# Kernel tuning notes

Measured on AMD Instinct MI355X. Metric: run time of the kernel, lower is better.

The kernel has to match this reference:

```python
import jax, jax.numpy as jnp
import numpy as np

C = 512
GROUPS = 32
EPS = 1e-6


def setup_inputs() -> dict:
    key = jax.random.key(0)
    ks = jax.random.split(key, 10)
    s = 0.02
    return {
        "x": jax.random.normal(ks[0], (2, C, 64, 64), dtype=jnp.float32),
        "gn_scale": jnp.ones((C,), jnp.float32),
        "gn_bias": jnp.zeros((C,), jnp.float32),
        "wq": jax.random.normal(ks[1], (C, C), jnp.float32) * s,
        "bq": jnp.zeros((C,), jnp.float32),
        "wk": jax.random.normal(ks[2], (C, C), jnp.float32) * s,
        "bk": jnp.zeros((C,), jnp.float32),
        "wv": jax.random.normal(ks[3], (C, C), jnp.float32) * s,
        "bv": jnp.zeros((C,), jnp.float32),
        "wo": jax.random.normal(ks[4], (C, C), jnp.float32) * s,
        "bo": jnp.zeros((C,), jnp.float32),
    }


def group_norm(x, scale, bias):
    # x: [b, c, h, w]; 32 groups over channel dim
    b, c, h, w = x.shape
    xg = x.reshape(b, GROUPS, c // GROUPS, h, w)
    mean = jnp.mean(xg, axis=(2, 3, 4), keepdims=True)
    var = jnp.var(xg, axis=(2, 3, 4), keepdims=True)
    xg = (xg - mean) * jax.lax.rsqrt(var + EPS)
    x = xg.reshape(b, c, h, w)
    return x * scale[None, :, None, None] + bias[None, :, None, None]


def reference(x, gn_scale, gn_bias, wq, bq, wk, bk, wv, bv, wo, bo):
    b, c, h, w = x.shape
    n = h * w
    hn = group_norm(x, gn_scale, gn_bias).reshape(b, c, n)  # [b,c,n]
    # 1x1 conv == channel matmul: out[b,o,n] = W[o,i] @ h[b,i,n] + bias
    q = jnp.einsum('oi,bin->bon', wq, hn) + bq[None, :, None]
    k = jnp.einsum('oi,bin->bon', wk, hn) + bk[None, :, None]
    v = jnp.einsum('oi,bin->bon', wv, hn) + bv[None, :, None]
    # weight[b, i, j] = q_i . k_j, softmax over j
    scale = int(c) ** (-0.5)
    weight = jnp.einsum('bci,bcj->bij', q, k) * scale  # [b,n,n]
    weight = jax.nn.softmax(weight, axis=2)
    # h[b,c,i] = sum_j v[b,c,j] * weight[b,i,j]
    out = jnp.einsum('bcj,bij->bci', v, weight)
    out = jnp.einsum('oi,bin->bon', wo, out) + bo[None, :, None]
    return out.reshape(b, c, h, w) + x
```

## Files before the change

### kernel.cpp

```cpp
#include <hip/hip_runtime.h>
#include <hip/hip_bf16.h>


typedef __attribute__((ext_vector_type(8))) short short8_t;
typedef __attribute__((ext_vector_type(4))) short short4_t;
typedef __attribute__((ext_vector_type(4))) float f32x4;

__device__ __forceinline__ void gload16(const void* g, void* l) {
  __builtin_amdgcn_global_load_lds(
      (const __attribute__((address_space(1))) void*)g,
      (__attribute__((address_space(3))) void*)l, 16, 0, 0);
}

__device__ __forceinline__ short f2bf_bits(float f) {
  __hip_bfloat16 h = __float2bfloat16(f);
  return *reinterpret_cast<short*>(&h);
}
__device__ __forceinline__ float bfbits2f(short s) {
  union { unsigned int u; float f; } c;
  c.u = ((unsigned int)(unsigned short)s) << 16;
  return c.f;
}

template<int OUTF, int BIASMODE, int RESID, int PIPE, int SWZ, int MF>
__global__ __launch_bounds__(256, 2)
void gemm_nt(const __hip_bfloat16* __restrict__ A,
             const __hip_bfloat16* __restrict__ B,
             void* __restrict__ Cv,
             const float* __restrict__ bias,
             const float* __restrict__ resid,
             float scale, int M, int N, int K,
             int lda, int ldb, int ldc,
             long long strA, long long strB, long long strC, long long strR)
{
  int bm, bn, bz;
  if (SWZ == 0) {
    bm = blockIdx.x; bn = blockIdx.y; bz = blockIdx.z;
  } else if (SWZ == 2) {
    const int b = blockIdx.x;
    bz = b >> 10;
    const int b2 = b & 1023;
    const int xcd = b2 & 7, s = b2 >> 3;
    bm = (xcd >> 1) * 8 + (s & 7);
    bn = (xcd & 1) * 16 + (s >> 3);
  } else {
    const int b = blockIdx.x;
    const int xcd = b & 7, slot = b >> 3;
    bm = slot & 7;
    const int panel = xcd * 8 + (slot >> 3);
    bn = panel & 31; bz = panel >> 5;
  }
  const int z = bz;
  A += (size_t)z * strA;
  B += (size_t)z * strB;

  const int tid = threadIdx.x;
  const int w = tid >> 6, l = tid & 63;
  const int wr = w >> 1, wc = w & 1;
  const int lhi = l >> 4, llo = l & 15;
  const int m0 = bm * (MF * 32), n0 = bn * 128;

  constexpr int BUFSZ = MF * 4096 + 16384;
  __shared__ char sm[(PIPE ? 2 : 1) * BUFSZ];

  f32x4 acc[MF][4] = {};

  const int rowInCh = l >> 3;
  const int colOff = 8 * ((l & 7) ^ (rowInCh & 7));

  const __hip_bfloat16* gAr[MF];
  const __hip_bfloat16* gBr[4];
#pragma unroll
  for (int j = 0; j < MF; ++j)
    gAr[j] = A + (size_t)(m0 + w * (8 * MF) + j * 8 + rowInCh) * lda + colOff;
#pragma unroll
  for (int r = 0; r < 4; ++r)
    gBr[r] = B + (size_t)(n0 + w * 32 + r * 8 + rowInCh) * ldb + colOff;

  auto stage = [&](int kt, int buf) {
    char* sA = sm + buf * BUFSZ;
    char* sB = sA + MF * 4096;
    const int ko = kt * 64;
#pragma unroll
    for (int j = 0; j < MF; ++j)
      gload16(gAr[j] + ko, sA + (w * MF + j) * 1024);
#pragma unroll
    for (int r = 0; r < 4; ++r)
      gload16(gBr[r] + ko, sB + (w * 4 + r) * 1024);
  };

  auto compute = [&](int buf) {
    char* sA = sm + buf * BUFSZ;
    char* sB = sA + MF * 4096;
#pragma unroll
    for (int kk = 0; kk < 2; ++kk) {
      short8_t af[MF], bf[4];
#pragma unroll
      for (int m = 0; m < MF; ++m) {
        const int row = wr * (16 * MF) + m * 16 + llo;
        const int inner = ((kk * 4 + lhi) ^ (row & 7)) * 16;
        af[m] = *(const short8_t*)(sA + row * 128 + inner);
      }
#pragma unroll
      for (int n = 0; n < 4; ++n) {
        const int row = wc * 64 + n * 16 + llo;
        const int inner = ((kk * 4 + lhi) ^ (row & 7)) * 16;
        bf[n] = *(const short8_t*)(sB + row * 128 + inner);
      }
#pragma unroll
      for (int m = 0; m < MF; ++m)
#pragma unroll
        for (int n = 0; n < 4; ++n)
          acc[m][n] = __builtin_amdgcn_mfma_f32_16x16x32_bf16(af[m], bf[n], acc[m][n], 0, 0, 0);
    }
  };

  const int nkt = K >> 6;
  if (PIPE) {
    stage(0, 0);
    __syncthreads();
    int cur = 0;
    for (int kt = 0; kt < nkt; ++kt) {
      if (kt + 1 < nkt) stage(kt + 1, cur ^ 1);
      compute(cur);
      __syncthreads();
      cur ^= 1;
    }
  } else {
    for (int kt = 0; kt < nkt; ++kt) {
      __syncthreads();
      stage(kt, 0);
      __syncthreads();
      compute(0);
    }
  }

#pragma unroll
  for (int m = 0; m < MF; ++m) {
#pragma unroll
    for (int r = 0; r < 4; ++r) {
      const int grow = m0 + wr * (16 * MF) + m * 16 + lhi * 4 + r;
#pragma unroll
      for (int n = 0; n < 4; ++n) {
        const int gcol = n0 + wc * 64 + n * 16 + llo;
        float v = acc[m][n][r] * scale;
        if (BIASMODE == 1) v += bias[grow];
        if (BIASMODE == 2) v += bias[gcol];
        const size_t idx = (size_t)z * strC + (size_t)grow * ldc + gcol;
        if (RESID) v += resid[(size_t)z * strR + (size_t)grow * ldc + gcol];
        if (OUTF == 0) ((__hip_bfloat16*)Cv)[idx] = __float2bfloat16(v);
        else           ((float*)Cv)[idx] = v;
      }
    }
  }
}

__global__ __launch_bounds__(256)
void gn_partial(const float* __restrict__ x, float* __restrict__ part)
{
  const int g = blockIdx.x, sl = blockIdx.y, z = blockIdx.z;
  const int tid = threadIdx.x;
  const float* xf = x + (size_t)z * 512 * 4096 + (size_t)g * 16 * 4096 + (size_t)sl * 4096;
  const float4* px = reinterpret_cast<const float4*>(xf);
  float s = 0.f, q = 0.f;
#pragma unroll
  for (int i = 0; i < 4; ++i) {
    float4 v = px[tid + i * 256];
    s += v.x + v.y + v.z + v.w;
    q += v.x * v.x + v.y * v.y + v.z * v.z + v.w * v.w;
  }
#pragma unroll
  for (int o = 32; o; o >>= 1) { s += __shfl_xor(s, o); q += __shfl_xor(q, o); }
  __shared__ float rs[4], rq[4];
  if ((tid & 63) == 0) { rs[tid >> 6] = s; rq[tid >> 6] = q; }
  __syncthreads();
  if (tid == 0) {
    s = rs[0] + rs[1] + rs[2] + rs[3];
    q = rq[0] + rq[1] + rq[2] + rq[3];
    part[(((size_t)z * 32 + g) * 16 + sl) * 2 + 0] = s;
    part[(((size_t)z * 32 + g) * 16 + sl) * 2 + 1] = q;
  }
}

__global__ __launch_bounds__(64)
void gn_finalize(const float* __restrict__ part, float* __restrict__ stats, int n)
{
  const int i = threadIdx.x;
  if (i >= n) return;
  float s = 0.f, q = 0.f;
#pragma unroll
  for (int sl = 0; sl < 16; ++sl) {
    s += part[(i * 16 + sl) * 2 + 0];
    q += part[(i * 16 + sl) * 2 + 1];
  }
  const float mean = s * (1.0f / 65536.0f);
  const float var = q * (1.0f / 65536.0f) - mean * mean;
  stats[i * 2 + 0] = mean;
  stats[i * 2 + 1] = rsqrtf(var + 1e-6f);
}

__global__ __launch_bounds__(256)
void gn_apply_t(const float* __restrict__ x, const float* __restrict__ stats,
                const float* __restrict__ gns, const float* __restrict__ gnb,
                __hip_bfloat16* __restrict__ ht)
{
  const int st = blockIdx.x, ct = blockIdx.y, z = blockIdx.z;
  const int tid = threadIdx.x;
  __shared__ float tile[64][65];
  const float* xb = x + (size_t)z * 512 * 4096;
  const int lane64 = tid & 63, rr = tid >> 6;
#pragma unroll
  for (int pp = 0; pp < 16; ++pp) {
    const int cl = pp * 4 + rr;
    const int c = ct * 64 + cl;
    const int g = c >> 4;
    const float mean = stats[(z * 32 + g) * 2 + 0];
    const float rstd = stats[(z * 32 + g) * 2 + 1];
    const float val = xb[(size_t)c * 4096 + st * 64 + lane64];
    tile[cl][lane64] = (val - mean) * rstd * gns[c] + gnb[c];
  }
  __syncthreads();
  __hip_bfloat16* hb = ht + (size_t)z * 4096 * 512;
#pragma unroll
  for (int pp = 0; pp < 16; ++pp) {
    const int sl = pp * 4 + rr;
    const int s = st * 64 + sl;
    hb[(size_t)s * 512 + ct * 64 + lane64] = __float2bfloat16(tile[lane64][sl]);
  }
}

__global__ __launch_bounds__(256)
void softmax_rows(__hip_bfloat16* __restrict__ S, long long strZ)
{
  const int row = blockIdx.x, z = blockIdx.y;
  __hip_bfloat16* p = S + (size_t)z * strZ + (size_t)row * 4096;
  const int tid = threadIdx.x;
  short8_t a = *(const short8_t*)(p + tid * 16);
  short8_t b = *(const short8_t*)(p + tid * 16 + 8);
  float v[16];
#pragma unroll
  for (int i = 0; i < 8; ++i) { v[i] = bfbits2f(a[i]); v[8 + i] = bfbits2f(b[i]); }
  float m = v[0];
#pragma unroll
  for (int i = 1; i < 16; ++i) m = fmaxf(m, v[i]);
#pragma unroll
  for (int o = 32; o; o >>= 1) m = fmaxf(m, __shfl_xor(m, o));
  __shared__ float red[8];
  if ((tid & 63) == 0) red[tid >> 6] = m;
  __syncthreads();
  m = fmaxf(fmaxf(red[0], red[1]), fmaxf(red[2], red[3]));
  float s = 0.f;
#pragma unroll
  for (int i = 0; i < 16; ++i) { v[i] = exp2f((v[i] - m) * 1.44269504f); s += v[i]; }
#pragma unroll
  for (int o = 32; o; o >>= 1) s += __shfl_xor(s, o);
  __syncthreads();
  if ((tid & 63) == 0) red[4 + (tid >> 6)] = s;
  __syncthreads();
  s = red[4] + red[5] + red[6] + red[7];
  const float inv = 1.f / s;
#pragma unroll
  for (int i = 0; i < 8; ++i) { a[i] = f2bf_bits(v[i] * inv); b[i] = f2bf_bits(v[8 + i] * inv); }
  *(short8_t*)(p + tid * 16) = a;
  *(short8_t*)(p + tid * 16 + 8) = b;
}

__global__ __launch_bounds__(256)
void cast3(const float* __restrict__ w0, const float* __restrict__ w1,
           const float* __restrict__ w2, __hip_bfloat16* __restrict__ out)
{
  const int j = blockIdx.y;
  const float* src = (j == 0) ? w0 : (j == 1) ? w1 : w2;
  const int i = blockIdx.x * 256 + threadIdx.x;
  float4 v = reinterpret_cast<const float4*>(src)[i];
  short4_t o;
  o[0] = f2bf_bits(v.x); o[1] = f2bf_bits(v.y);
  o[2] = f2bf_bits(v.z); o[3] = f2bf_bits(v.w);
  *reinterpret_cast<short4_t*>((short*)out + (size_t)j * 262144 + (size_t)i * 4) = o;
}

__global__ __launch_bounds__(256)
void transpose_cast(const float* __restrict__ w, __hip_bfloat16* __restrict__ wt)
{
  __shared__ float tile[64][65];
  const int ct = blockIdx.x, it = blockIdx.y;
  const int tid = threadIdx.x;
  const int lane = tid & 63, rr = tid >> 6;
#pragma unroll
  for (int p = 0; p < 16; ++p) {
    const int cl = p * 4 + rr;
    tile[cl][lane] = w[(size_t)(ct * 64 + cl) * 512 + it * 64 + lane];
  }
  __syncthreads();
#pragma unroll
  for (int p = 0; p < 16; ++p) {
    const int il = p * 4 + rr;
    wt[(size_t)(it * 64 + il) * 512 + ct * 64 + lane] = __float2bfloat16(tile[lane][il]);
  }
}

__global__ __launch_bounds__(64)
void prep_bias(const float* __restrict__ wo, const float* __restrict__ bv,
               const float* __restrict__ bo, const float* __restrict__ bq,
               const float* __restrict__ bk,
               float* __restrict__ bvo, float* __restrict__ bqk)
{
  const int o = blockIdx.x * 64 + threadIdx.x;
  const float4* row = reinterpret_cast<const float4*>(wo + (size_t)o * 512);
  const float4* b4 = reinterpret_cast<const float4*>(bv);
  float s = 0.f;
#pragma unroll 8
  for (int i = 0; i < 128; ++i) {
    float4 a = row[i], b = b4[i];
    s += a.x * b.x + a.y * b.y + a.z * b.z + a.w * b.w;
  }
  bvo[o] = s + bo[o];
  bqk[o] = bq[o];
  bqk[512 + o] = bk[o];
}

extern "C" void kernel_launch(void* const* d_in, const int* in_sizes, int n_in,
                              void* d_out, int out_size, void* d_ws, size_t ws_size,
                              hipStream_t stream)
{
  const float* x   = (const float*)d_in[0];
  const float* gns = (const float*)d_in[1];
  const float* gnb = (const float*)d_in[2];
  const float* wq  = (const float*)d_in[3];
  const float* bq  = (const float*)d_in[4];
  const float* wk  = (const float*)d_in[5];
  const float* bk  = (const float*)d_in[6];
  const float* wv  = (const float*)d_in[7];
  const float* bv  = (const float*)d_in[8];
  const float* wo  = (const float*)d_in[9];
  const float* bo  = (const float*)d_in[10];
  float* out = (float*)d_out;

  const int WB = 512 * 512;
  const long long HT  = 4096LL * 512;
  const long long QKz = 4096LL * 1024;
  const long long VOz = 512LL * 4096;
  const long long SS  = 4096LL * 4096;
  const long long CHW = 512LL * 4096;

  char* base = (char*)d_ws;
  size_t off = 0;
  auto alloc = [&](size_t b) { void* r = base + off; off = (off + b + 255) & ~(size_t)255; return r; };

  __hip_bfloat16* wbf = (__hip_bfloat16*)alloc((size_t)5 * WB * 2);
  float* bqk   = (float*)alloc(1024 * 4);
  float* bvo   = (float*)alloc(512 * 4);
  float* part  = (float*)alloc(2 * 32 * 16 * 2 * 4);
  float* stats = (float*)alloc(2 * 32 * 2 * 4);
  const size_t fixed = off;

  const size_t qkB = (size_t)2 * QKz * 2;
  const size_t voB = (size_t)2 * VOz * 2;
  const size_t sB2 = (size_t)2 * SS * 2;
  const size_t sB1 = (size_t)SS * 2;
  const int MODE = (ws_size >= fixed + qkB + voB + sB2) ? 2 : 1;

  __hip_bfloat16* qk   = (__hip_bfloat16*)alloc(qkB);
  __hip_bfloat16* vo   = (__hip_bfloat16*)alloc(voB);
  const size_t sbufB = (MODE == 2) ? sB2 : sB1;
  __hip_bfloat16* sbuf = (__hip_bfloat16*)alloc(sbufB);
  __hip_bfloat16* ht = (__hip_bfloat16*)((char*)sbuf + sbufB - (size_t)2 * HT * 2);

  __hip_bfloat16* wqk = wbf;
  __hip_bfloat16* woB = wbf + 2 * WB;
  __hip_bfloat16* wvT = wbf + 3 * WB;
  __hip_bfloat16* wvo = wbf + 4 * WB;

  const float SC = 0.04419417382415922f;

  cast3<<<dim3(256, 3), 256, 0, stream>>>(wq, wk, wo, wbf);
  transpose_cast<<<dim3(8, 8), 256, 0, stream>>>(wv, wvT);
  prep_bias<<<8, 64, 0, stream>>>(wo, bv, bo, bq, bk, bvo, bqk);
  gn_partial<<<dim3(32, 16, 2), 256, 0, stream>>>(x, part);
  gn_finalize<<<1, 64, 0, stream>>>(part, stats, 64);

  gemm_nt<0, 0, 0, 1, 0, 4><<<dim3(4, 4, 1), 256, 0, stream>>>(
      woB, wvT, wvo, nullptr, nullptr, 1.f, 512, 512, 512,
      512, 512, 512, 0, 0, 0, 0);

  gn_apply_t<<<dim3(64, 8, 2), 256, 0, stream>>>(x, stats, gns, gnb, ht);

  gemm_nt<0, 2, 0, 1, 0, 4><<<dim3(32, 8, 2), 256, 0, stream>>>(
      ht, wqk, qk, bqk, nullptr, 1.f, 4096, 1024, 512,
      512, 512, 1024, HT, 0, QKz, 0);

  gemm_nt<0, 0, 0, 1, 3, 2><<<dim3(512, 1, 1), 256, 0, stream>>>(
      wvo, ht, vo, nullptr, nullptr, 1.f, 512, 4096, 512,
      512, 512, 4096, 0, HT, VOz, 0);

  if (MODE == 2) {
    gemm_nt<0, 0, 0, 0, 2, 4><<<dim3(2048, 1, 1), 256, 0, stream>>>(
        qk, qk + 512, sbuf, nullptr, nullptr, SC, 4096, 4096, 512,
        1024, 1024, 4096, QKz, QKz, SS, 0);
    softmax_rows<<<dim3(4096, 2), 256, 0, stream>>>(sbuf, SS);
    gemm_nt<1, 1, 1, 1, 3, 2><<<dim3(512, 1, 1), 256, 0, stream>>>(
        vo, sbuf, out, bvo, x, 1.f, 512, 4096, 4096,
        4096, 4096, 4096, VOz, SS, CHW, CHW);
  } else {
    for (int z = 0; z < 2; ++z) {
      gemm_nt<0, 0, 0, 0, 0, 4><<<dim3(32, 32, 1), 256, 0, stream>>>(
          qk + (size_t)z * QKz, qk + (size_t)z * QKz + 512, sbuf, nullptr, nullptr,
          SC, 4096, 4096, 512, 1024, 1024, 4096, 0, 0, 0, 0);
      softmax_rows<<<dim3(4096, 1), 256, 0, stream>>>(sbuf, 0);
      gemm_nt<1, 1, 1, 1, 0, 2><<<dim3(8, 32, 1), 256, 0, stream>>>(
          vo + (size_t)z * VOz, sbuf, out + (size_t)z * CHW, bvo, x + (size_t)z * CHW,
          1.f, 512, 4096, 4096, 4096, 4096, 4096, 0, 0, 0, 0);
    }
  }
}
```

Baseline: 167.6 us.

## Add triple-buffered LDS pipeline with vmcnt waits and new XCD swizzle for scores GEMM

Adds a PIPE==2 mode to the GEMM that keeps three LDS buffers and prefetches two k-tiles ahead. It waits with s_waitcnt vmcnt on the outstanding async loads plus a single barrier per iteration, instead of a full sync after each compute. The QK^T scores GEMM switches from MF=4 with the old swizzle and no pipelining to MF=2 with a new XCD-aware block mapping over 4096 blocks. The aim is to hide global-to-LDS latency and improve L2 locality, at the cost of extra shared memory, which may reduce occupancy.

```diff
diff --git a/kernel.cpp b/kernel.cpp
--- a/kernel.cpp
+++ b/kernel.cpp
@@ -36,19 +36,19 @@
   int bm, bn, bz;
   if (SWZ == 0) {
     bm = blockIdx.x; bn = blockIdx.y; bz = blockIdx.z;
-  } else if (SWZ == 2) {
-    const int b = blockIdx.x;
-    bz = b >> 10;
-    const int b2 = b & 1023;
-    const int xcd = b2 & 7, s = b2 >> 3;
-    bm = (xcd >> 1) * 8 + (s & 7);
-    bn = (xcd & 1) * 16 + (s >> 3);
-  } else {
+  } else if (SWZ == 3) {
     const int b = blockIdx.x;
     const int xcd = b & 7, slot = b >> 3;
     bm = slot & 7;
     const int panel = xcd * 8 + (slot >> 3);
     bn = panel & 31; bz = panel >> 5;
+  } else {
+    const int b = blockIdx.x;
+    const int xcd = b & 7;
+    const int s = b >> 3;
+    bz = xcd >> 2;
+    bm = (xcd & 3) * 16 + (s & 15);
+    bn = s >> 4;
   }
   const int z = bz;
   A += (size_t)z * strA;
@@ -61,7 +61,9 @@
   const int m0 = bm * (MF * 32), n0 = bn * 128;
 
   constexpr int BUFSZ = MF * 4096 + 16384;
-  __shared__ char sm[(PIPE ? 2 : 1) * BUFSZ];
+  constexpr int NBUF = (PIPE == 2) ? 3 : (PIPE == 1) ? 2 : 1;
+  constexpr int LOADS = MF + 4;
+  __shared__ char sm[NBUF * BUFSZ];
 
   f32x4 acc[MF][4] = {};
 
@@ -116,7 +118,25 @@
   };
 
   const int nkt = K >> 6;
-  if (PIPE) {
+  if (PIPE == 2) {
+    stage(0, 0);
+    if (nkt > 1) stage(1, 1);
+    int cur = 0;
+    for (int kt = 0; kt < nkt; ++kt) {
+      if (kt + 1 < nkt) {
+        asm volatile("s_waitcnt vmcnt(%0)" :: "n"(LOADS) : "memory");
+      } else {
+        asm volatile("s_waitcnt vmcnt(0)" ::: "memory");
+      }
+      __builtin_amdgcn_sched_barrier(0);
+      __builtin_amdgcn_s_barrier();
+      __builtin_amdgcn_sched_barrier(0);
+      int st = cur + 2; if (st >= 3) st -= 3;
+      if (kt + 2 < nkt) stage(kt + 2, st);
+      compute(cur);
+      ++cur; if (cur == 3) cur = 0;
+    }
+  } else if (PIPE == 1) {
     stage(0, 0);
     __syncthreads();
     int cur = 0;
@@ -389,16 +409,16 @@
       ht, wqk, qk, bqk, nullptr, 1.f, 4096, 1024, 512,
       512, 512, 1024, HT, 0, QKz, 0);
 
-  gemm_nt<0, 0, 0, 1, 3, 2><<<dim3(512, 1, 1), 256, 0, stream>>>(
+  gemm_nt<0, 0, 0, 2, 3, 2><<<dim3(512, 1, 1), 256, 0, stream>>>(
       wvo, ht, vo, nullptr, nullptr, 1.f, 512, 4096, 512,
       512, 512, 4096, 0, HT, VOz, 0);
 
   if (MODE == 2) {
-    gemm_nt<0, 0, 0, 0, 2, 4><<<dim3(2048, 1, 1), 256, 0, stream>>>(
+    gemm_nt<0, 0, 0, 2, 4, 2><<<dim3(4096, 1, 1), 256, 0, stream>>>(
         qk, qk + 512, sbuf, nullptr, nullptr, SC, 4096, 4096, 512,
         1024, 1024, 4096, QKz, QKz, SS, 0);
     softmax_rows<<<dim3(4096, 2), 256, 0, stream>>>(sbuf, SS);
-    gemm_nt<1, 1, 1, 1, 3, 2><<<dim3(512, 1, 1), 256, 0, stream>>>(
+    gemm_nt<1, 1, 1, 2, 3, 2><<<dim3(512, 1, 1), 256, 0, stream>>>(
         vo, sbuf, out, bvo, x, 1.f, 512, 4096, 4096,
         4096, 4096, 4096, VOz, SS, CHW, CHW);
   } else {
```

New measurement: 173.2 us. 1.03x slower.

## Add dedicated 256x256-tile 8-wave QK^T score GEMM with phased LDS pipeline

Applied to the files above, without the earlier changes.

Replaces the generic gemm_nt call for the attention score matrix with a specialized kernel that uses 256x256 output tiles, 512 threads, a double-buffered 128KB LDS with XOR swizzle, and fine-grained phases that interleave global-to-LDS loads with MFMA work under setprio. A block index remap groups tiles by XCD for L2 locality. The larger tile cuts global traffic per FLOP. In exchange it relies on high register use, occupancy of one block per CU, and scalar bf16 stores in the epilogue.

```diff
diff --git a/kernel.cpp b/kernel.cpp
--- a/kernel.cpp
+++ b/kernel.cpp
@@ -20,6 +20,117 @@
   union { unsigned int u; float f; } c;
   c.u = ((unsigned int)(unsigned short)s) << 16;
   return c.f;
+}
+
+__global__ __launch_bounds__(512)
+void s_gemm8(const __hip_bfloat16* __restrict__ qk,
+             __hip_bfloat16* __restrict__ S, float scale)
+{
+  const long long QKz = 4096LL * 1024;
+  const long long SS  = 4096LL * 4096;
+
+  const int b = blockIdx.x;
+  const int bz = b >> 8;
+  const int r = b & 255, xcd = r & 7, sl = r >> 3;
+  const int bm = (xcd >> 1) * 4 + (sl & 3);
+  const int bn = (xcd & 1) * 8 + (sl >> 2);
+
+  const __hip_bfloat16* Aq = qk + (size_t)bz * QKz;
+  const __hip_bfloat16* Bk = Aq + 512;
+
+  const int tid = threadIdx.x;
+  const int wid = tid >> 6, l = tid & 63;
+  const int wrM = wid >> 2, wcN = wid & 3;
+  const int lhi = l >> 4, llo = l & 15;
+
+  __shared__ char sm[2 * 65536];
+
+  f32x4 acc[2][2][4][2] = {};
+
+  const int rIn = l >> 3;
+  const int colSw = 8 * ((l & 7) ^ (rIn & 7));
+  const __hip_bfloat16* gA = Aq + (size_t)(bm * 256 + rIn) * 1024 + colSw;
+  const __hip_bfloat16* gB = Bk + (size_t)(bn * 256 + rIn) * 1024 + colSw;
+
+  auto STG = [&](int mat, int half, int t) {
+    const __hip_bfloat16* src = mat ? gB : gA;
+    char* dst = sm + (t & 1) * 65536 + mat * 32768;
+    const int rb = half * 128 + wid * 16;
+    gload16(src + (size_t)rb * 1024 + t * 64, dst + rb * 128);
+    gload16(src + (size_t)(rb + 8) * 1024 + t * 64, dst + (rb + 8) * 128);
+  };
+
+#define PHASE(MH, NH, RBUF, ...) do {                                         \
+    asm volatile("s_waitcnt vmcnt(4)" ::: "memory");                          \
+    __builtin_amdgcn_sched_barrier(0);                                        \
+    short8_t af[4][2], bf[2][2];                                              \
+    const char* bbA = sm + (RBUF) * 65536;                                    \
+    const char* bbB = bbA + 32768;                                            \
+    _Pragma("unroll") for (int m = 0; m < 4; ++m) {                           \
+      const int rowA = (MH) * 128 + wrM * 64 + m * 16 + llo;                  \
+      _Pragma("unroll") for (int kk = 0; kk < 2; ++kk)                        \
+        af[m][kk] = *(const short8_t*)(bbA + rowA * 128 +                     \
+                      (((kk * 4 + lhi) ^ (rowA & 7)) * 16));                  \
+    }                                                                         \
+    _Pragma("unroll") for (int n = 0; n < 2; ++n) {                           \
+      const int rowB = (NH) * 128 + wcN * 32 + n * 16 + llo;                  \
+      _Pragma("unroll") for (int kk = 0; kk < 2; ++kk)                        \
+        bf[n][kk] = *(const short8_t*)(bbB + rowB * 128 +                     \
+                      (((kk * 4 + lhi) ^ (rowB & 7)) * 16));                  \
+    }                                                                         \
+    __VA_ARGS__;                                                              \
+    __builtin_amdgcn_sched_barrier(0);                                        \
+    __builtin_amdgcn_s_barrier();                                             \
+    __builtin_amdgcn_sched_barrier(0);                                        \
+    __builtin_amdgcn_s_setprio(1);                                            \
+    _Pragma("unroll") for (int kk = 0; kk < 2; ++kk)                          \
+      _Pragma("unroll") for (int m = 0; m < 4; ++m)                           \
+        _Pragma("unroll") for (int n = 0; n < 2; ++n)                         \
+          acc[MH][NH][m][n] = __builtin_amdgcn_mfma_f32_16x16x32_bf16(        \
+              af[m][kk], bf[n][kk], acc[MH][NH][m][n], 0, 0, 0);              \
+    __builtin_amdgcn_s_setprio(0);                                            \
+    __builtin_amdgcn_sched_barrier(0);                                        \
+    __builtin_amdgcn_s_barrier();                                             \
+    __builtin_amdgcn_sched_barrier(0);                                        \
+  } while (0)
+
+  STG(0, 0, 0); STG(1, 0, 0); STG(0, 1, 0); STG(1, 1, 0);
+  STG(0, 0, 1); STG(1, 0, 1); STG(0, 1, 1); STG(1, 1, 1);
+  asm volatile("s_waitcnt vmcnt(0)" ::: "memory");
+  __builtin_amdgcn_sched_barrier(0);
+  __builtin_amdgcn_s_barrier();
+  __builtin_amdgcn_sched_barrier(0);
+
+  for (int i = 0; i < 4; ++i) {
+    const int t1 = 2 * i + 1, t2 = 2 * i + 2, t3 = 2 * i + 3;
+    PHASE(0, 0, 0, if (i >= 1) STG(0, 1, t1));
+    PHASE(0, 1, 0, if (i >= 1) STG(1, 1, t1));
+    PHASE(1, 0, 0, if (t2 < 8) STG(0, 0, t2));
+    PHASE(1, 1, 0, if (t2 < 8) STG(1, 0, t2));
+    PHASE(0, 0, 1, if (t2 < 8) STG(0, 1, t2));
+    PHASE(0, 1, 1, if (t2 < 8) STG(1, 1, t2));
+    PHASE(1, 0, 1, if (t3 < 8) STG(0, 0, t3));
+    PHASE(1, 1, 1, if (t3 < 8) STG(1, 0, t3));
+  }
+#undef PHASE
+
+  __hip_bfloat16* Sb = S + (size_t)bz * SS;
+#pragma unroll
+  for (int Mh = 0; Mh < 2; ++Mh)
+#pragma unroll
+    for (int m = 0; m < 4; ++m)
+#pragma unroll
+      for (int rr = 0; rr < 4; ++rr) {
+        const int grow = bm * 256 + Mh * 128 + wrM * 64 + m * 16 + lhi * 4 + rr;
+#pragma unroll
+        for (int Nh = 0; Nh < 2; ++Nh)
+#pragma unroll
+          for (int n = 0; n < 2; ++n) {
+            const int gcol = bn * 256 + Nh * 128 + wcN * 32 + n * 16 + llo;
+            Sb[(size_t)grow * 4096 + gcol] =
+                __float2bfloat16(acc[Mh][Nh][m][n][rr] * scale);
+          }
+      }
 }
 
 template<int OUTF, int BIASMODE, int RESID, int PIPE, int SWZ, int MF>
@@ -394,9 +505,7 @@
       512, 512, 4096, 0, HT, VOz, 0);
 
   if (MODE == 2) {
-    gemm_nt<0, 0, 0, 0, 2, 4><<<dim3(2048, 1, 1), 256, 0, stream>>>(
-        qk, qk + 512, sbuf, nullptr, nullptr, SC, 4096, 4096, 512,
-        1024, 1024, 4096, QKz, QKz, SS, 0);
+    s_gemm8<<<512, 512, 0, stream>>>(qk, sbuf, SC);
     softmax_rows<<<dim3(4096, 2), 256, 0, stream>>>(sbuf, SS);
     gemm_nt<1, 1, 1, 1, 3, 2><<<dim3(512, 1, 1), 256, 0, stream>>>(
         vo, sbuf, out, bvo, x, 1.f, 512, 4096, 4096,
```

Result: slower. 172.3 us (+2.8%).
